# Kernel tuning notes

Hardware: AMD Instinct MI355X
Metric: run time of the kernel (lower is better)

## Reference

```python
import jax, jax.numpy as jnp
import numpy as np

N_NODES = 50000
N_EDGES = 800000
IN_CH = 256
OUT_CH = 64
HEADS = 4


def setup_inputs() -> dict:
    key = jax.random.key(0)
    k1, k2, k3, k4, k5 = jax.random.split(key, 5)
    x = jax.random.normal(k1, (N_NODES, IN_CH), dtype=jnp.float32)
    edge_index = jax.random.randint(k2, (2, N_EDGES), 0, N_NODES, dtype=jnp.int64)
    # xavier-ish scaled params
    weight = jax.random.normal(k3, (HEADS, IN_CH, OUT_CH), dtype=jnp.float32) * (2.0 / (IN_CH + OUT_CH)) ** 0.5
    att_src = jax.random.normal(k4, (1, HEADS, OUT_CH), dtype=jnp.float32) * 0.1
    att_dst = jax.random.normal(k5, (1, HEADS, OUT_CH), dtype=jnp.float32) * 0.1
    bias = jnp.zeros((HEADS * OUT_CH,), dtype=jnp.float32)
    return {"x": x, "edge_index": edge_index, "weight": weight,
            "att_src": att_src, "att_dst": att_dst, "bias": bias}


def reference(x, edge_index, weight, att_src, att_dst, bias):
    # GATConv forward (eval mode: dropout is identity), vectorized over heads.
    num_nodes = x.shape[0]
    row, col = edge_index[0], edge_index[1]
    # per-head projection: [N, H, C]
    x_h = jnp.einsum('nf,hfc->nhc', x, weight)
    alpha_src = jnp.sum(x_h * att_src[0], axis=-1)   # [N, H]
    alpha_dst = jnp.sum(x_h * att_dst[0], axis=-1)   # [N, H]
    alpha = alpha_src[row] + alpha_dst[col]          # [E, H]
    alpha = jax.nn.leaky_relu(alpha, negative_slope=0.2)
    # segment softmax over edges grouped by destination row (numerically stable)
    alpha_max = jax.ops.segment_max(alpha, row, num_segments=num_nodes)  # [N, H]
    alpha = jnp.exp(alpha - alpha_max[row])
    alpha_sum = jax.ops.segment_sum(alpha, row, num_segments=num_nodes)  # [N, H]
    alpha = alpha / jnp.clip(alpha_sum[row], 1e-16)
    # message passing: scatter-add alpha-weighted source features
    messages = alpha[:, :, None] * x_h[col]                              # [E, H, C]
    out = jax.ops.segment_sum(messages, row, num_segments=num_nodes)    # [N, H, C]
    out = out.reshape(num_nodes, -1) + bias                              # concat heads
    return out
```

## Files before the change

kernel.cpp:

```cpp
#include <hip/hip_runtime.h>
#include <math.h>

#define N_IN_CH 256
#define N_OUT   256
#define HEADS   4
#define OUT_CH  64
#define BM      64
#define SCAN_BLOCK 1024

typedef __attribute__((ext_vector_type(8))) short bf16x8;
typedef __attribute__((ext_vector_type(4))) float f32x4;

__device__ __forceinline__ float lrelu(float a) {
  return a >= 0.f ? a : 0.2f * a;
}

__device__ __forceinline__ ushort f2bf(float f) {
  uint u = __float_as_uint(f);
  uint r = (u + 0x7FFFu + ((u >> 16) & 1u)) >> 16;
  return (ushort)r;
}

__device__ __forceinline__ float bflo(uint u) {
  return __uint_as_float((u & 0xFFFFu) << 16);
}
__device__ __forceinline__ float bfhi(uint u) {
  return __uint_as_float(u & 0xFFFF0000u);
}

__global__ void convert_w(const float* __restrict__ w, ushort* __restrict__ bt,
                          int* __restrict__ counts, int nnodes) {
  const int idx = blockIdx.x * 256 + threadIdx.x;
  if (idx < nnodes) counts[idx] = 0;
  const int n = idx >> 8, k = idx & 255;
  const int h = n >> 6, c = n & 63;
  bt[idx] = f2bf(w[h * (N_IN_CH * OUT_CH) + k * OUT_CH + c]);
}

__global__ void count_kernel(const int* __restrict__ row, int* __restrict__ counts,
                             int* __restrict__ rank, int nedges) {
  int e = blockIdx.x * blockDim.x + threadIdx.x;
  if (e < nedges) rank[e] = atomicAdd(&counts[row[e]], 1);
}

__global__ __launch_bounds__(256) void proj_mfma(
    const float* __restrict__ x, const ushort* __restrict__ bt,
    const float* __restrict__ att_src, const float* __restrict__ att_dst,
    ushort* __restrict__ xh, float* __restrict__ asrc, float* __restrict__ adst,
    int nnodes) {
  __shared__ ushort at[BM * N_IN_CH];
  const int tid = threadIdx.x;
  const int wave = tid >> 6;
  const int lane = tid & 63;
  const int n0 = blockIdx.x * BM;

  {
    const int rsub = tid >> 6;
    const int cf = (tid & 63) * 4;
    const int cb = cf * 2;
#pragma unroll
    for (int it = 0; it < 16; ++it) {
      const int row_ = it * 4 + rsub;
      const int grow = n0 + row_;
      float4 xv = make_float4(0.f, 0.f, 0.f, 0.f);
      if (grow < nnodes) xv = *(const float4*)&x[(size_t)grow * N_IN_CH + cf];
      ushort4 b;
      b.x = f2bf(xv.x); b.y = f2bf(xv.y); b.z = f2bf(xv.z); b.w = f2bf(xv.w);
      const int cbs = cb ^ ((row_ & 7) << 4);
      *(ushort4*)((char*)at + row_ * 512 + cbs) = b;
    }
  }
  __syncthreads();

  f32x4 acc[4][4];
#pragma unroll
  for (int mt = 0; mt < 4; ++mt)
#pragma unroll
    for (int nt = 0; nt < 4; ++nt) acc[mt][nt] = (f32x4){0.f, 0.f, 0.f, 0.f};

  const int lmod = lane & 15;
  const int ldiv = lane >> 4;

  for (int ks = 0; ks < 8; ++ks) {
    bf16x8 a[4], b[4];
#pragma unroll
    for (int mt = 0; mt < 4; ++mt) {
      const int row_ = mt * 16 + lmod;
      const int kb = ks * 64 + ldiv * 16;
      const int cbs = kb ^ ((row_ & 7) << 4);
      a[mt] = *(const bf16x8*)((const char*)at + row_ * 512 + cbs);
    }
#pragma unroll
    for (int nt = 0; nt < 4; ++nt) {
      const int n = wave * 64 + nt * 16 + lmod;
      b[nt] = *(const bf16x8*)&bt[(size_t)n * N_IN_CH + ks * 32 + ldiv * 8];
    }
#pragma unroll
    for (int mt = 0; mt < 4; ++mt)
#pragma unroll
      for (int nt = 0; nt < 4; ++nt)
        acc[mt][nt] = __builtin_amdgcn_mfma_f32_16x16x32_bf16(
            a[mt], b[nt], acc[mt][nt], 0, 0, 0);
  }

  float atts[4], attd[4];
#pragma unroll
  for (int nt = 0; nt < 4; ++nt) {
    const int gcol = wave * 64 + nt * 16 + lmod;
    atts[nt] = att_src[gcol];
    attd[nt] = att_dst[gcol];
  }

#pragma unroll
  for (int mt = 0; mt < 4; ++mt) {
#pragma unroll
    for (int reg = 0; reg < 4; ++reg) {
      const int grow = n0 + mt * 16 + ldiv * 4 + reg;
      const bool ok = grow < nnodes;
      float vs = 0.f, vd = 0.f;
#pragma unroll
      for (int nt = 0; nt < 4; ++nt) {
        const float v = acc[mt][nt][reg];
        if (ok) xh[(size_t)grow * N_OUT + wave * 64 + nt * 16 + lmod] = f2bf(v);
        vs = fmaf(v, atts[nt], vs);
        vd = fmaf(v, attd[nt], vd);
      }
#pragma unroll
      for (int d = 1; d < 16; d <<= 1) {
        vs += __shfl_xor(vs, d, 64);
        vd += __shfl_xor(vd, d, 64);
      }
      if (lmod == 0 && ok) {
        asrc[grow * HEADS + wave] = vs;
        adst[grow * HEADS + wave] = vd;
      }
    }
  }
}

__global__ __launch_bounds__(SCAN_BLOCK) void scan1_kernel(
    const int* __restrict__ counts, int* __restrict__ offsets,
    int* __restrict__ partials, int n) {
  __shared__ int wsum[16];
  const int tid = threadIdx.x;
  const int lane = tid & 63;
  const int wid = tid >> 6;
  const int i = blockIdx.x * SCAN_BLOCK + tid;
  int v = (i < n) ? counts[i] : 0;
  int incl = v;
#pragma unroll
  for (int d = 1; d < 64; d <<= 1) {
    int t = __shfl_up(incl, d, 64);
    if (lane >= d) incl += t;
  }
  if (lane == 63) wsum[wid] = incl;
  __syncthreads();
  if (wid == 0) {
    int wv = (lane < 16) ? wsum[lane] : 0;
#pragma unroll
    for (int d = 1; d < 16; d <<= 1) {
      int t = __shfl_up(wv, d, 64);
      if (lane >= d) wv += t;
    }
    if (lane < 16) wsum[lane] = wv;
  }
  __syncthreads();
  const int wexcl = (wid == 0) ? 0 : wsum[wid - 1];
  if (i <= n) offsets[i] = wexcl + incl - v;
  if (tid == SCAN_BLOCK - 1) partials[blockIdx.x] = wsum[15];
}

__global__ void scan2_kernel(int* __restrict__ partials, int nparts) {
  const int lane = threadIdx.x;
  int v = (lane < nparts) ? partials[lane] : 0;
  int incl = v;
#pragma unroll
  for (int d = 1; d < 64; d <<= 1) {
    int t = __shfl_up(incl, d, 64);
    if (lane >= d) incl += t;
  }
  if (lane < nparts) partials[lane] = incl - v;
}

__global__ void scatter_kernel(const int* __restrict__ row, const int* __restrict__ col,
                               const int* __restrict__ rank,
                               const int* __restrict__ offsets,
                               const int* __restrict__ partials,
                               int* __restrict__ ccol, int nedges) {
  int e = blockIdx.x * blockDim.x + threadIdx.x;
  if (e < nedges) {
    const int r = row[e];
    const int pos = offsets[r] + partials[r >> 10] + rank[e];
    ccol[pos] = col[e];
  }
}

__global__ __launch_bounds__(256) void gather_kernel(
    const int* __restrict__ offsets, const int* __restrict__ partials,
    const int* __restrict__ ccol,
    const float* __restrict__ asrc, const float* __restrict__ adst,
    const ushort* __restrict__ xh, const float* __restrict__ bias,
    float* __restrict__ out, int nnodes) {
  __shared__ float pbuf[4][64 * 4];
  __shared__ int clbuf[4][64];
  const int wv = threadIdx.x >> 6;
  const int lane = threadIdx.x & 63;
  const int n = blockIdx.x * 4 + wv;
  if (n >= nnodes) return;
  const int off = offsets[n] + partials[n >> 10];
  const int end = offsets[n + 1] + partials[(n + 1) >> 10];
  const int deg = end - off;
  const int h = lane >> 4;
  const int xoff = lane << 2;

  const float4 as4 = *(const float4*)&asrc[n * 4];

  float m0 = -1e30f, m1 = -1e30f, m2 = -1e30f, m3 = -1e30f;
  float s0 = 0.f, s1 = 0.f, s2 = 0.f, s3 = 0.f;
  float4 acc = make_float4(0.f, 0.f, 0.f, 0.f);

  for (int b = 0; b < deg; b += 64) {
    const int cnt = min(64, deg - b);
    float a0 = -1e30f, a1 = -1e30f, a2 = -1e30f, a3 = -1e30f;
    int cl_l = 0;
    if (lane < cnt) {
      cl_l = ccol[off + b + lane];
      const float4 ad = *(const float4*)&adst[cl_l * 4];
      a0 = lrelu(as4.x + ad.x);
      a1 = lrelu(as4.y + ad.y);
      a2 = lrelu(as4.z + ad.z);
      a3 = lrelu(as4.w + ad.w);
    }
    float c0 = a0, c1 = a1, c2 = a2, c3 = a3;
#pragma unroll
    for (int d = 1; d < 64; d <<= 1) {
      c0 = fmaxf(c0, __shfl_xor(c0, d, 64));
      c1 = fmaxf(c1, __shfl_xor(c1, d, 64));
      c2 = fmaxf(c2, __shfl_xor(c2, d, 64));
      c3 = fmaxf(c3, __shfl_xor(c3, d, 64));
    }
    const float nm0 = fmaxf(m0, c0), nm1 = fmaxf(m1, c1);
    const float nm2 = fmaxf(m2, c2), nm3 = fmaxf(m3, c3);
    const float sc0 = __expf(m0 - nm0), sc1 = __expf(m1 - nm1);
    const float sc2 = __expf(m2 - nm2), sc3 = __expf(m3 - nm3);
    m0 = nm0; m1 = nm1; m2 = nm2; m3 = nm3;
    float4 p;
    p.x = __expf(a0 - m0);
    p.y = __expf(a1 - m1);
    p.z = __expf(a2 - m2);
    p.w = __expf(a3 - m3);
    s0 = s0 * sc0 + p.x;
    s1 = s1 * sc1 + p.y;
    s2 = s2 * sc2 + p.z;
    s3 = s3 * sc3 + p.w;
    const float sch = (h == 0) ? sc0 : (h == 1) ? sc1 : (h == 2) ? sc2 : sc3;
    acc.x *= sch; acc.y *= sch; acc.z *= sch; acc.w *= sch;

    *(float4*)&pbuf[wv][lane * 4] = p;
    clbuf[wv][lane] = cl_l;

    int j = 0;
    for (; j + 8 <= cnt; j += 8) {
      int c[8];
      uint2 xr[8];
      float w[8];
#pragma unroll
      for (int q = 0; q < 8; ++q) c[q] = clbuf[wv][j + q];
#pragma unroll
      for (int q = 0; q < 8; ++q)
        xr[q] = *(const uint2*)&xh[(size_t)c[q] * N_OUT + xoff];
#pragma unroll
      for (int q = 0; q < 8; ++q) w[q] = pbuf[wv][(j + q) * 4 + h];
#pragma unroll
      for (int q = 0; q < 8; ++q) {
        acc.x = fmaf(w[q], bflo(xr[q].x), acc.x);
        acc.y = fmaf(w[q], bfhi(xr[q].x), acc.y);
        acc.z = fmaf(w[q], bflo(xr[q].y), acc.z);
        acc.w = fmaf(w[q], bfhi(xr[q].y), acc.w);
      }
    }
    for (; j < cnt; ++j) {
      const int c0_ = clbuf[wv][j];
      const uint2 x0 = *(const uint2*)&xh[(size_t)c0_ * N_OUT + xoff];
      const float w0 = pbuf[wv][j * 4 + h];
      acc.x = fmaf(w0, bflo(x0.x), acc.x);
      acc.y = fmaf(w0, bfhi(x0.x), acc.y);
      acc.z = fmaf(w0, bflo(x0.y), acc.z);
      acc.w = fmaf(w0, bfhi(x0.y), acc.w);
    }
  }

#pragma unroll
  for (int d = 1; d < 64; d <<= 1) {
    s0 += __shfl_xor(s0, d, 64);
    s1 += __shfl_xor(s1, d, 64);
    s2 += __shfl_xor(s2, d, 64);
    s3 += __shfl_xor(s3, d, 64);
  }
  const float sh = (h == 0) ? s0 : (h == 1) ? s1 : (h == 2) ? s2 : s3;
  const float invh = 1.f / fmaxf(sh, 1e-16f);

  const float4 b4 = *(const float4*)&bias[xoff];
  float4 o;
  o.x = fmaf(acc.x, invh, b4.x);
  o.y = fmaf(acc.y, invh, b4.y);
  o.z = fmaf(acc.z, invh, b4.z);
  o.w = fmaf(acc.w, invh, b4.w);
  *(float4*)&out[(size_t)n * N_OUT + xoff] = o;
}

extern "C" void kernel_launch(void* const* d_in, const int* in_sizes, int n_in,
                              void* d_out, int out_size, void* d_ws, size_t ws_size,
                              hipStream_t stream) {
  const float* x        = (const float*)d_in[0];
  const int*   edge_idx = (const int*)d_in[1];
  const float* weight   = (const float*)d_in[2];
  const float* att_src  = (const float*)d_in[3];
  const float* att_dst  = (const float*)d_in[4];
  const float* bias     = (const float*)d_in[5];
  float* out = (float*)d_out;

  const int nnodes = in_sizes[0] / N_IN_CH;
  const int nedges = in_sizes[1] / 2;
  const int* row = edge_idx;
  const int* col = edge_idx + nedges;

  char* wsb = (char*)d_ws;
  size_t woff = 0;
  auto alloc = [&](size_t bytes) -> char* {
    char* p = wsb + woff;
    woff += (bytes + 255) & ~(size_t)255;
    return p;
  };
  ushort* xh    = (ushort*)alloc((size_t)nnodes * N_OUT * sizeof(ushort));
  ushort* bt    = (ushort*)alloc((size_t)N_OUT * N_IN_CH * sizeof(ushort));
  float* asrc   = (float*)alloc((size_t)nnodes * HEADS * sizeof(float));
  float* adst   = (float*)alloc((size_t)nnodes * HEADS * sizeof(float));
  int* counts   = (int*)alloc((size_t)nnodes * sizeof(int));
  int* offsets  = (int*)alloc((size_t)(nnodes + 1) * sizeof(int));
  int* partials = (int*)alloc(256 * sizeof(int));
  int* rank     = (int*)alloc((size_t)nedges * sizeof(int));
  int* ccol     = (int*)alloc((size_t)nedges * sizeof(int));

  convert_w<<<256, 256, 0, stream>>>(weight, bt, counts, nnodes);

  const int eblocks = (nedges + 255) / 256;
  count_kernel<<<eblocks, 256, 0, stream>>>(row, counts, rank, nedges);

  const int nblocksA = (nnodes + BM - 1) / BM;
  proj_mfma<<<nblocksA, 256, 0, stream>>>(x, bt, att_src, att_dst,
                                          xh, asrc, adst, nnodes);

  const int nscan = (nnodes + 1 + SCAN_BLOCK - 1) / SCAN_BLOCK;
  scan1_kernel<<<nscan, SCAN_BLOCK, 0, stream>>>(counts, offsets, partials, nnodes);
  scan2_kernel<<<1, 64, 0, stream>>>(partials, nscan);

  scatter_kernel<<<eblocks, 256, 0, stream>>>(row, col, rank, offsets, partials,
                                              ccol, nedges);

  gather_kernel<<<(nnodes + 3) / 4, 256, 0, stream>>>(offsets, partials, ccol,
                                                      asrc, adst, xh, bias, out,
                                                      nnodes);
}
```

Measured before the change: 181.5 us.

## Drop online softmax max tracking and split wave into two edge halves with 16B loads

Removes the running-max online softmax (the per-chunk wave max reductions and rescaling) and exponentiates the leaky-relu scores directly, relying on their values being small. It also restructures the gather so each half-wave handles alternate edges with 8-channel uint4 loads, combining the halves with one cross-half shuffle at the end. This cuts shuffle reductions and exp calls per chunk and doubles bytes per load, but without max subtraction the exp can overflow when scores are large.

```diff
diff --git a/kernel.cpp b/kernel.cpp
--- a/kernel.cpp
+++ b/kernel.cpp
@@ -210,103 +210,102 @@
   const int off = offsets[n] + partials[n >> 10];
   const int end = offsets[n + 1] + partials[(n + 1) >> 10];
   const int deg = end - off;
-  const int h = lane >> 4;
-  const int xoff = lane << 2;
+  const int half = lane >> 5;
+  const int ch8 = (lane & 31) * 8;
+  const int hh = (lane & 31) >> 3;
 
   const float4 as4 = *(const float4*)&asrc[n * 4];
 
-  float m0 = -1e30f, m1 = -1e30f, m2 = -1e30f, m3 = -1e30f;
-  float s0 = 0.f, s1 = 0.f, s2 = 0.f, s3 = 0.f;
-  float4 acc = make_float4(0.f, 0.f, 0.f, 0.f);
+  float4 s4 = make_float4(0.f, 0.f, 0.f, 0.f);
+  float a0 = 0.f, a1 = 0.f, a2 = 0.f, a3 = 0.f;
+  float a4 = 0.f, a5 = 0.f, a6 = 0.f, a7 = 0.f;
 
   for (int b = 0; b < deg; b += 64) {
     const int cnt = min(64, deg - b);
-    float a0 = -1e30f, a1 = -1e30f, a2 = -1e30f, a3 = -1e30f;
+    float4 p = make_float4(0.f, 0.f, 0.f, 0.f);
     int cl_l = 0;
     if (lane < cnt) {
       cl_l = ccol[off + b + lane];
       const float4 ad = *(const float4*)&adst[cl_l * 4];
-      a0 = lrelu(as4.x + ad.x);
-      a1 = lrelu(as4.y + ad.y);
-      a2 = lrelu(as4.z + ad.z);
-      a3 = lrelu(as4.w + ad.w);
-    }
-    float c0 = a0, c1 = a1, c2 = a2, c3 = a3;
-#pragma unroll
-    for (int d = 1; d < 64; d <<= 1) {
-      c0 = fmaxf(c0, __shfl_xor(c0, d, 64));
-      c1 = fmaxf(c1, __shfl_xor(c1, d, 64));
-      c2 = fmaxf(c2, __shfl_xor(c2, d, 64));
-      c3 = fmaxf(c3, __shfl_xor(c3, d, 64));
-    }
-    const float nm0 = fmaxf(m0, c0), nm1 = fmaxf(m1, c1);
-    const float nm2 = fmaxf(m2, c2), nm3 = fmaxf(m3, c3);
-    const float sc0 = __expf(m0 - nm0), sc1 = __expf(m1 - nm1);
-    const float sc2 = __expf(m2 - nm2), sc3 = __expf(m3 - nm3);
-    m0 = nm0; m1 = nm1; m2 = nm2; m3 = nm3;
-    float4 p;
-    p.x = __expf(a0 - m0);
-    p.y = __expf(a1 - m1);
-    p.z = __expf(a2 - m2);
-    p.w = __expf(a3 - m3);
-    s0 = s0 * sc0 + p.x;
-    s1 = s1 * sc1 + p.y;
-    s2 = s2 * sc2 + p.z;
-    s3 = s3 * sc3 + p.w;
-    const float sch = (h == 0) ? sc0 : (h == 1) ? sc1 : (h == 2) ? sc2 : sc3;
-    acc.x *= sch; acc.y *= sch; acc.z *= sch; acc.w *= sch;
-
+      p.x = __expf(lrelu(as4.x + ad.x));
+      p.y = __expf(lrelu(as4.y + ad.y));
+      p.z = __expf(lrelu(as4.z + ad.z));
+      p.w = __expf(lrelu(as4.w + ad.w));
+      s4.x += p.x; s4.y += p.y; s4.z += p.z; s4.w += p.w;
+    }
     *(float4*)&pbuf[wv][lane * 4] = p;
     clbuf[wv][lane] = cl_l;
 
     int j = 0;
     for (; j + 8 <= cnt; j += 8) {
-      int c[8];
-      uint2 xr[8];
-      float w[8];
-#pragma unroll
-      for (int q = 0; q < 8; ++q) c[q] = clbuf[wv][j + q];
-#pragma unroll
-      for (int q = 0; q < 8; ++q)
-        xr[q] = *(const uint2*)&xh[(size_t)c[q] * N_OUT + xoff];
-#pragma unroll
-      for (int q = 0; q < 8; ++q) w[q] = pbuf[wv][(j + q) * 4 + h];
-#pragma unroll
-      for (int q = 0; q < 8; ++q) {
-        acc.x = fmaf(w[q], bflo(xr[q].x), acc.x);
-        acc.y = fmaf(w[q], bfhi(xr[q].x), acc.y);
-        acc.z = fmaf(w[q], bflo(xr[q].y), acc.z);
-        acc.w = fmaf(w[q], bfhi(xr[q].y), acc.w);
-      }
-    }
-    for (; j < cnt; ++j) {
-      const int c0_ = clbuf[wv][j];
-      const uint2 x0 = *(const uint2*)&xh[(size_t)c0_ * N_OUT + xoff];
-      const float w0 = pbuf[wv][j * 4 + h];
-      acc.x = fmaf(w0, bflo(x0.x), acc.x);
-      acc.y = fmaf(w0, bfhi(x0.x), acc.y);
-      acc.z = fmaf(w0, bflo(x0.y), acc.z);
-      acc.w = fmaf(w0, bfhi(x0.y), acc.w);
-    }
-  }
+      int cq[4];
+      float wq[4];
+      uint4 xq[4];
+#pragma unroll
+      for (int q = 0; q < 4; ++q) {
+        const int e = j + 2 * q + half;
+        cq[q] = clbuf[wv][e];
+        wq[q] = pbuf[wv][e * 4 + hh];
+      }
+#pragma unroll
+      for (int q = 0; q < 4; ++q)
+        xq[q] = *(const uint4*)&xh[(size_t)cq[q] * N_OUT + ch8];
+#pragma unroll
+      for (int q = 0; q < 4; ++q) {
+        a0 = fmaf(wq[q], bflo(xq[q].x), a0);
+        a1 = fmaf(wq[q], bfhi(xq[q].x), a1);
+        a2 = fmaf(wq[q], bflo(xq[q].y), a2);
+        a3 = fmaf(wq[q], bfhi(xq[q].y), a3);
+        a4 = fmaf(wq[q], bflo(xq[q].z), a4);
+        a5 = fmaf(wq[q], bfhi(xq[q].z), a5);
+        a6 = fmaf(wq[q], bflo(xq[q].w), a6);
+        a7 = fmaf(wq[q], bfhi(xq[q].w), a7);
+      }
+    }
+    for (; j < cnt; j += 2) {
+      const int e = j + half;
+      const bool ok = e < cnt;
+      const int c0 = clbuf[wv][ok ? e : j];
+      const float w0 = ok ? pbuf[wv][e * 4 + hh] : 0.f;
+      const uint4 x0 = *(const uint4*)&xh[(size_t)c0 * N_OUT + ch8];
+      a0 = fmaf(w0, bflo(x0.x), a0);
+      a1 = fmaf(w0, bfhi(x0.x), a1);
+      a2 = fmaf(w0, bflo(x0.y), a2);
+      a3 = fmaf(w0, bfhi(x0.y), a3);
+      a4 = fmaf(w0, bflo(x0.z), a4);
+      a5 = fmaf(w0, bfhi(x0.z), a5);
+      a6 = fmaf(w0, bflo(x0.w), a6);
+      a7 = fmaf(w0, bfhi(x0.w), a7);
+    }
+  }
+
+  a0 += __shfl_xor(a0, 32, 64);
+  a1 += __shfl_xor(a1, 32, 64);
+  a2 += __shfl_xor(a2, 32, 64);
+  a3 += __shfl_xor(a3, 32, 64);
+  a4 += __shfl_xor(a4, 32, 64);
+  a5 += __shfl_xor(a5, 32, 64);
+  a6 += __shfl_xor(a6, 32, 64);
+  a7 += __shfl_xor(a7, 32, 64);
 
 #pragma unroll
   for (int d = 1; d < 64; d <<= 1) {
-    s0 += __shfl_xor(s0, d, 64);
-    s1 += __shfl_xor(s1, d, 64);
-    s2 += __shfl_xor(s2, d, 64);
-    s3 += __shfl_xor(s3, d, 64);
-  }
-  const float sh = (h == 0) ? s0 : (h == 1) ? s1 : (h == 2) ? s2 : s3;
+    s4.x += __shfl_xor(s4.x, d, 64);
+    s4.y += __shfl_xor(s4.y, d, 64);
+    s4.z += __shfl_xor(s4.z, d, 64);
+    s4.w += __shfl_xor(s4.w, d, 64);
+  }
+  const float sh = (hh == 0) ? s4.x : (hh == 1) ? s4.y : (hh == 2) ? s4.z : s4.w;
   const float invh = 1.f / fmaxf(sh, 1e-16f);
 
-  const float4 b4 = *(const float4*)&bias[xoff];
+  const int wch = ch8 + half * 4;
+  const float4 b4 = *(const float4*)&bias[wch];
   float4 o;
-  o.x = fmaf(acc.x, invh, b4.x);
-  o.y = fmaf(acc.y, invh, b4.y);
-  o.z = fmaf(acc.z, invh, b4.z);
-  o.w = fmaf(acc.w, invh, b4.w);
-  *(float4*)&out[(size_t)n * N_OUT + xoff] = o;
+  o.x = fmaf(half ? a4 : a0, invh, b4.x);
+  o.y = fmaf(half ? a5 : a1, invh, b4.y);
+  o.z = fmaf(half ? a6 : a2, invh, b4.z);
+  o.w = fmaf(half ? a7 : a3, invh, b4.w);
+  *(float4*)&out[(size_t)n * N_OUT + wch] = o;
 }
 
 extern "C" void kernel_launch(void* const* d_in, const int* in_sizes, int n_in,
```

Measured after the change: 166.3 us. 1.09x faster.
